# Optimization experiments

Measured on AMD Instinct MI355X. Metric: run time of the kernel, lower is better.

Reference implementation:

```python
import jax, jax.numpy as jnp
import numpy as np

B, P, C = 64, 8732, 81
NEG_POS_RATIO = 3


def _smooth_l1_masked_sum(p, t, maskf):
    # smooth_l1 with beta=1, sum reduction, restricted to positive priors
    d = jnp.abs(p - t)
    l = jnp.where(d < 1.0, 0.5 * d * d, d - 0.5)  # [B,P,K]
    return jnp.sum(l.sum(-1) * maskf)


def setup_inputs() -> dict:
    key = jax.random.key(0)
    ks = jax.random.split(key, 6)
    loc_data = jax.random.normal(ks[0], (B, P, 4), jnp.float32)
    conf_data = jax.random.normal(ks[1], (B, P, C), jnp.float32)
    four_corners_data = jax.random.normal(ks[2], (B, P, 8), jnp.float32)
    loc_t = jax.random.normal(ks[3], (B, P, 4), jnp.float32)
    four_corners_t = jax.random.normal(ks[4], (B, P, 8), jnp.float32)
    conf_t = jax.random.randint(ks[5], (B, P), 0, C, jnp.int32)
    return {
        "loc_data": loc_data,
        "conf_data": conf_data,
        "four_corners_data": four_corners_data,
        "loc_t": loc_t,
        "four_corners_t": four_corners_t,
        "conf_t": conf_t,
    }


def reference(loc_data, conf_data, four_corners_data, loc_t, four_corners_t, conf_t):
    num_priors = conf_data.shape[1]
    pos = conf_t > 0                                  # [B,P]
    posf = pos.astype(conf_data.dtype)

    # localization + four-corner smooth-L1 over matched (positive) priors
    loss_l = _smooth_l1_masked_sum(loc_data, loc_t, posf)
    loss_four_corners = _smooth_l1_masked_sum(four_corners_data, four_corners_t, posf)

    # per-prior CE loss: log_sum_exp(conf) - conf[target]
    lse = jax.nn.logsumexp(conf_data, axis=-1)        # [B,P]
    gathered = jnp.take_along_axis(conf_data, conf_t[..., None], axis=-1)[..., 0]
    ce_all = lse - gathered                           # [B,P]

    # hard-negative mining: rank negatives by CE loss (double argsort)
    loss_c_mine = jnp.where(pos, 0.0, ce_all)
    loss_idx = jnp.argsort(-loss_c_mine, axis=1)      # descending sort indices
    idx_rank = jnp.argsort(loss_idx, axis=1)          # rank of each prior
    num_pos = pos.sum(axis=1, keepdims=True)          # [B,1]
    num_neg = jnp.minimum(NEG_POS_RATIO * num_pos, num_priors - 1)
    neg = idx_rank < num_neg                          # [B,P]

    sel = pos | neg
    loss_c = jnp.sum(jnp.where(sel, ce_all, 0.0))

    N = num_pos.sum().astype(conf_data.dtype)
    return (loss_l / N, loss_c / N, loss_four_corners / N)
```

## Files before the change

### kernel.cpp

```cpp
#include <hip/hip_runtime.h>


#define NB 64
#define NP 8732
#define NC 81
constexpr int BP = NB * NP;
constexpr int PBLK = (NP + 255) / 256;
constexpr unsigned MAXCH = (unsigned)((size_t)BP * NC / 4 - 1);

__device__ inline float sl1(float d) {
    d = fabsf(d);
    return d < 1.0f ? 0.5f * d * d : d - 0.5f;
}


__global__ __launch_bounds__(256) void k_main(
    const float* __restrict__ loc_data, const float* __restrict__ conf_data,
    const float* __restrict__ fc_data,  const float* __restrict__ loc_t,
    const float* __restrict__ fc_t,     const int* __restrict__ conf_t,
    float* __restrict__ ce, float* __restrict__ part)
{
    const int b  = blockIdx.y;
    const int bx = blockIdx.x;
    const int t  = threadIdx.x;
    const int p0 = bx << 8;

    __shared__ int   tgt_s[256];
    __shared__ float red[4][5];

    float l_sum = 0.0f, f_sum = 0.0f, sp = 0.0f, sn = 0.0f;
    int np = 0;

    {
        const int p = p0 + t;
        int tgt = 0;
        if (p < NP) {
            const size_t g = (size_t)b * NP + p;
            tgt = conf_t[g];
            const float posf = (tgt > 0) ? 1.0f : 0.0f;
            np = (tgt > 0) ? 1 : 0;
            float4 a4  = ((const float4*)loc_data)[g];
            float4 a4t = ((const float4*)loc_t)[g];
            l_sum = (sl1(a4.x - a4t.x) + sl1(a4.y - a4t.y) +
                     sl1(a4.z - a4t.z) + sl1(a4.w - a4t.w)) * posf;
            float4 c0 = ((const float4*)fc_data)[2 * g];
            float4 c1 = ((const float4*)fc_data)[2 * g + 1];
            float4 d0 = ((const float4*)fc_t)[2 * g];
            float4 d1 = ((const float4*)fc_t)[2 * g + 1];
            f_sum = (sl1(c0.x - d0.x) + sl1(c0.y - d0.y) + sl1(c0.z - d0.z) + sl1(c0.w - d0.w) +
                     sl1(c1.x - d1.x) + sl1(c1.y - d1.y) + sl1(c1.z - d1.z) + sl1(c1.w - d1.w)) * posf;
        }
        tgt_s[t] = tgt;
    }
    __syncthreads();

    const int wave = t >> 6, lane = t & 63;
    const int grp = lane >> 2, sub = lane & 3;
    const float4* conf4 = (const float4*)conf_data;

    #pragma unroll 1
    for (int s = 0; s < 4; ++s) {
        const int pl = (wave << 6) + (s << 4) + grp;
        const int p  = p0 + pl;
        const int pe = min(p, NP - 1);
        const unsigned g  = (unsigned)b * NP + (unsigned)pe;
        const unsigned fb = g * (unsigned)NC;
        const int al      = (int)(fb & 3u);
        const unsigned c0 = fb >> 2;

        const int tgt = tgt_s[pl];
        float tv = 0.0f;
        if (sub == 0) tv = conf_data[fb + (unsigned)tgt];

        float e = 0.0f;
        #pragma unroll
        for (int k = 0; k < 6; ++k) {
            unsigned ch = c0 + (unsigned)(sub + 4 * k);
            ch = ch > MAXCH ? MAXCH : ch;
            const float4 v = conf4[ch];
            const int bi = 4 * (sub + 4 * k) - al;
            e += ((unsigned)(bi + 0) < 81u) ? __expf(v.x) : 0.0f;
            e += ((unsigned)(bi + 1) < 81u) ? __expf(v.y) : 0.0f;
            e += ((unsigned)(bi + 2) < 81u) ? __expf(v.z) : 0.0f;
            e += ((unsigned)(bi + 3) < 81u) ? __expf(v.w) : 0.0f;
        }
        e += __shfl_xor(e, 1, 64);
        e += __shfl_xor(e, 2, 64);

        if (sub == 0 && p < NP) {
            const float cev = __logf(e) - tv;
            ce[g] = cev;
            if (tgt > 0) sp += cev; else sn += cev;
        }
    }

    float vnp = (float)np;
    #pragma unroll
    for (int o = 32; o; o >>= 1) {
        l_sum += __shfl_xor(l_sum, o, 64);
        f_sum += __shfl_xor(f_sum, o, 64);
        sp    += __shfl_xor(sp, o, 64);
        sn    += __shfl_xor(sn, o, 64);
        vnp   += __shfl_xor(vnp, o, 64);
    }
    if (lane == 0) {
        red[wave][0] = l_sum; red[wave][1] = f_sum;
        red[wave][2] = sp;    red[wave][3] = sn;   red[wave][4] = vnp;
    }
    __syncthreads();
    if (t == 0) {
        float rl = 0, rf = 0, rp = 0, rn = 0, rc = 0;
        #pragma unroll
        for (int w = 0; w < 4; ++w) {
            rl += red[w][0]; rf += red[w][1]; rp += red[w][2];
            rn += red[w][3]; rc += red[w][4];
        }
        float* pp = part + ((size_t)b * PBLK + bx) * 5;
        pp[0] = rl; pp[1] = rf; pp[2] = rp; pp[3] = rn; pp[4] = rc;
    }
}

__global__ __launch_bounds__(256) void k_batch(
    const float* __restrict__ ce, const int* __restrict__ conf_t,
    const float* __restrict__ part, float* __restrict__ loss_c_b,
    int* __restrict__ npos_b, float* __restrict__ lsum_b, float* __restrict__ fsum_b)
{
    const int b = blockIdx.x;
    const int t = threadIdx.x;
    __shared__ float hdr[3];

    if (t < 64) {
        float v0 = 0, v1 = 0, v2 = 0, v3 = 0, v4 = 0;
        if (t < PBLK) {
            const float* pp = part + ((size_t)b * PBLK + t) * 5;
            v0 = pp[0]; v1 = pp[1]; v2 = pp[2]; v3 = pp[3]; v4 = pp[4];
        }
        #pragma unroll
        for (int o = 32; o; o >>= 1) {
            v0 += __shfl_xor(v0, o, 64);
            v1 += __shfl_xor(v1, o, 64);
            v2 += __shfl_xor(v2, o, 64);
            v3 += __shfl_xor(v3, o, 64);
            v4 += __shfl_xor(v4, o, 64);
        }
        if (t == 0) {
            lsum_b[b] = v0; fsum_b[b] = v1;
            npos_b[b] = (int)v4;
            hdr[0] = v2; hdr[1] = v3; hdr[2] = v4;
        }
    }
    __syncthreads();

    const float spos = hdr[0], sneg = hdr[1];
    const int npos    = (int)hdr[2];
    const int nneg    = NP - npos;
    const int num_neg = min(3 * npos, NP - 1);

    if (num_neg >= nneg) {
        if (t == 0) loss_c_b[b] = spos + sneg;
        return;
    }
    if (num_neg <= 0) {
        if (t == 0) loss_c_b[b] = spos;
        return;
    }

    __shared__ float ce_s[NP];
    __shared__ float sredf[4];
    __shared__ int   sredi[4];
    const float* crow = ce + (size_t)b * NP;
    const int*   trow = conf_t + (size_t)b * NP;
    for (int p = t; p < NP; p += 256)
        ce_s[p] = (trow[p] > 0) ? -1.0f : crow[p];
    __syncthreads();

    const int wave = t >> 6, lane = t & 63;
    const int K = num_neg;
    unsigned lo = 0u, hi = 0x7f800000u;
    while (lo < hi) {
        unsigned mid = lo + ((hi - lo) >> 1);
        float v = __uint_as_float(mid);
        int c_t = 0;
        for (int p = t; p < NP; p += 256) c_t += (ce_s[p] > v) ? 1 : 0;
        #pragma unroll
        for (int o = 32; o; o >>= 1) c_t += __shfl_xor(c_t, o, 64);
        __syncthreads();
        if (lane == 0) sredi[wave] = c_t;
        __syncthreads();
        int cnt = sredi[0] + sredi[1] + sredi[2] + sredi[3];
        if (cnt < K) hi = mid; else lo = mid + 1;
    }
    float v = __uint_as_float(lo);
    int c_t = 0; float s_t = 0.0f;
    for (int p = t; p < NP; p += 256) {
        float x = ce_s[p];
        if (x > v) { c_t++; s_t += x; }
    }
    #pragma unroll
    for (int o = 32; o; o >>= 1) {
        c_t += __shfl_xor(c_t, o, 64);
        s_t += __shfl_xor(s_t, o, 64);
    }
    __syncthreads();
    if (lane == 0) { sredi[wave] = c_t; sredf[wave] = s_t; }
    __syncthreads();
    if (t == 0) {
        int   cnt = sredi[0] + sredi[1] + sredi[2] + sredi[3];
        float sgt = sredf[0] + sredf[1] + sredf[2] + sredf[3];
        loss_c_b[b] = spos + sgt + (float)(K - cnt) * v;
    }
}

__global__ void k_final(const float* __restrict__ loss_c_b,
                        const int* __restrict__ npos_b,
                        const float* __restrict__ lsum_b,
                        const float* __restrict__ fsum_b,
                        float* __restrict__ out)
{
    const int t = threadIdx.x;
    float lc = loss_c_b[t];
    float ls = lsum_b[t];
    float fs = fsum_b[t];
    int   np = npos_b[t];
    #pragma unroll
    for (int o = 32; o; o >>= 1) {
        lc += __shfl_xor(lc, o, 64);
        ls += __shfl_xor(ls, o, 64);
        fs += __shfl_xor(fs, o, 64);
        np += __shfl_xor(np, o, 64);
    }
    if (t == 0) {
        float N = (float)np;
        out[0] = ls / N;
        out[1] = lc / N;
        out[2] = fs / N;
    }
}

extern "C" void kernel_launch(void* const* d_in, const int* in_sizes, int n_in,
                              void* d_out, int out_size, void* d_ws, size_t ws_size,
                              hipStream_t stream)
{
    const float* loc_data  = (const float*)d_in[0];
    const float* conf_data = (const float*)d_in[1];
    const float* fc_data   = (const float*)d_in[2];
    const float* loc_t     = (const float*)d_in[3];
    const float* fc_t      = (const float*)d_in[4];
    const int*   conf_t    = (const int*)d_in[5];
    float* out = (float*)d_out;

    float* ce       = (float*)d_ws;
    float* part     = ce + BP;
    float* loss_c_b = part + NB * PBLK * 5;
    int*   npos_b   = (int*)(loss_c_b + 64);
    float* lsum_b   = (float*)(npos_b + 64);
    float* fsum_b   = lsum_b + 64;

    hipLaunchKernelGGL(k_main,  dim3(PBLK, NB), dim3(256), 0, stream,
                       loc_data, conf_data, fc_data, loc_t, fc_t, conf_t,
                       ce, part);
    hipLaunchKernelGGL(k_batch, dim3(NB), dim3(256), 0, stream,
                       ce, conf_t, part, loss_c_b, npos_b, lsum_b, fsum_b);
    hipLaunchKernelGGL(k_final, dim3(1), dim3(64), 0, stream,
                       loss_c_b, npos_b, lsum_b, fsum_b, out);
}
```

Measured before the change: 305.2 us.

## Split smooth-L1 and CE into separate kernels, double-buffer conf loads

The fused main kernel becomes two kernels: one for the smooth-L1 sums and positive count, one for per-prior cross-entropy. The CE kernel uses double-buffered register prefetch of the conf rows so loads for the next sub-tile are in flight while the current one is computed. It also takes the target logit from the already-loaded vectors instead of doing a separate scalar gather. The cost is an extra kernel launch, more registers, and reading conf_t twice.

```diff
diff --git a/kernel.cpp b/kernel.cpp
--- a/kernel.cpp
+++ b/kernel.cpp
@@ -14,116 +14,158 @@
 }
 
 
-__global__ __launch_bounds__(256) void k_main(
-    const float* __restrict__ loc_data, const float* __restrict__ conf_data,
-    const float* __restrict__ fc_data,  const float* __restrict__ loc_t,
-    const float* __restrict__ fc_t,     const int* __restrict__ conf_t,
-    float* __restrict__ ce, float* __restrict__ part)
+__global__ __launch_bounds__(256) void k_sl1(
+    const float* __restrict__ loc_data, const float* __restrict__ fc_data,
+    const float* __restrict__ loc_t,    const float* __restrict__ fc_t,
+    const int* __restrict__ conf_t,     float* __restrict__ partS)
 {
     const int b  = blockIdx.y;
     const int bx = blockIdx.x;
     const int t  = threadIdx.x;
-    const int p0 = bx << 8;
-
-    __shared__ int   tgt_s[256];
-    __shared__ float red[4][5];
-
-    float l_sum = 0.0f, f_sum = 0.0f, sp = 0.0f, sn = 0.0f;
+    const int p  = (bx << 8) + t;
+
+    __shared__ float red[4][3];
+    float l_sum = 0.0f, f_sum = 0.0f;
     int np = 0;
 
-    {
-        const int p = p0 + t;
-        int tgt = 0;
-        if (p < NP) {
-            const size_t g = (size_t)b * NP + p;
-            tgt = conf_t[g];
-            const float posf = (tgt > 0) ? 1.0f : 0.0f;
-            np = (tgt > 0) ? 1 : 0;
-            float4 a4  = ((const float4*)loc_data)[g];
-            float4 a4t = ((const float4*)loc_t)[g];
-            l_sum = (sl1(a4.x - a4t.x) + sl1(a4.y - a4t.y) +
-                     sl1(a4.z - a4t.z) + sl1(a4.w - a4t.w)) * posf;
-            float4 c0 = ((const float4*)fc_data)[2 * g];
-            float4 c1 = ((const float4*)fc_data)[2 * g + 1];
-            float4 d0 = ((const float4*)fc_t)[2 * g];
-            float4 d1 = ((const float4*)fc_t)[2 * g + 1];
-            f_sum = (sl1(c0.x - d0.x) + sl1(c0.y - d0.y) + sl1(c0.z - d0.z) + sl1(c0.w - d0.w) +
-                     sl1(c1.x - d1.x) + sl1(c1.y - d1.y) + sl1(c1.z - d1.z) + sl1(c1.w - d1.w)) * posf;
-        }
-        tgt_s[t] = tgt;
-    }
-    __syncthreads();
+    if (p < NP) {
+        const size_t g = (size_t)b * NP + p;
+        const int tgt = conf_t[g];
+        const float posf = (tgt > 0) ? 1.0f : 0.0f;
+        np = (tgt > 0) ? 1 : 0;
+        float4 a4  = ((const float4*)loc_data)[g];
+        float4 a4t = ((const float4*)loc_t)[g];
+        float4 c0  = ((const float4*)fc_data)[2 * g];
+        float4 c1  = ((const float4*)fc_data)[2 * g + 1];
+        float4 d0  = ((const float4*)fc_t)[2 * g];
+        float4 d1  = ((const float4*)fc_t)[2 * g + 1];
+        l_sum = (sl1(a4.x - a4t.x) + sl1(a4.y - a4t.y) +
+                 sl1(a4.z - a4t.z) + sl1(a4.w - a4t.w)) * posf;
+        f_sum = (sl1(c0.x - d0.x) + sl1(c0.y - d0.y) + sl1(c0.z - d0.z) + sl1(c0.w - d0.w) +
+                 sl1(c1.x - d1.x) + sl1(c1.y - d1.y) + sl1(c1.z - d1.z) + sl1(c1.w - d1.w)) * posf;
+    }
 
     const int wave = t >> 6, lane = t & 63;
-    const int grp = lane >> 2, sub = lane & 3;
-    const float4* conf4 = (const float4*)conf_data;
-
-    #pragma unroll 1
-    for (int s = 0; s < 4; ++s) {
-        const int pl = (wave << 6) + (s << 4) + grp;
-        const int p  = p0 + pl;
-        const int pe = min(p, NP - 1);
-        const unsigned g  = (unsigned)b * NP + (unsigned)pe;
-        const unsigned fb = g * (unsigned)NC;
-        const int al      = (int)(fb & 3u);
-        const unsigned c0 = fb >> 2;
-
-        const int tgt = tgt_s[pl];
-        float tv = 0.0f;
-        if (sub == 0) tv = conf_data[fb + (unsigned)tgt];
-
-        float e = 0.0f;
-        #pragma unroll
-        for (int k = 0; k < 6; ++k) {
-            unsigned ch = c0 + (unsigned)(sub + 4 * k);
-            ch = ch > MAXCH ? MAXCH : ch;
-            const float4 v = conf4[ch];
-            const int bi = 4 * (sub + 4 * k) - al;
-            e += ((unsigned)(bi + 0) < 81u) ? __expf(v.x) : 0.0f;
-            e += ((unsigned)(bi + 1) < 81u) ? __expf(v.y) : 0.0f;
-            e += ((unsigned)(bi + 2) < 81u) ? __expf(v.z) : 0.0f;
-            e += ((unsigned)(bi + 3) < 81u) ? __expf(v.w) : 0.0f;
-        }
-        e += __shfl_xor(e, 1, 64);
-        e += __shfl_xor(e, 2, 64);
-
-        if (sub == 0 && p < NP) {
-            const float cev = __logf(e) - tv;
-            ce[g] = cev;
-            if (tgt > 0) sp += cev; else sn += cev;
-        }
-    }
-
     float vnp = (float)np;
     #pragma unroll
     for (int o = 32; o; o >>= 1) {
         l_sum += __shfl_xor(l_sum, o, 64);
         f_sum += __shfl_xor(f_sum, o, 64);
-        sp    += __shfl_xor(sp, o, 64);
-        sn    += __shfl_xor(sn, o, 64);
         vnp   += __shfl_xor(vnp, o, 64);
     }
-    if (lane == 0) {
-        red[wave][0] = l_sum; red[wave][1] = f_sum;
-        red[wave][2] = sp;    red[wave][3] = sn;   red[wave][4] = vnp;
-    }
+    if (lane == 0) { red[wave][0] = l_sum; red[wave][1] = f_sum; red[wave][2] = vnp; }
     __syncthreads();
     if (t == 0) {
-        float rl = 0, rf = 0, rp = 0, rn = 0, rc = 0;
+        float rl = 0, rf = 0, rc = 0;
         #pragma unroll
-        for (int w = 0; w < 4; ++w) {
-            rl += red[w][0]; rf += red[w][1]; rp += red[w][2];
-            rn += red[w][3]; rc += red[w][4];
-        }
-        float* pp = part + ((size_t)b * PBLK + bx) * 5;
-        pp[0] = rl; pp[1] = rf; pp[2] = rp; pp[3] = rn; pp[4] = rc;
+        for (int w = 0; w < 4; ++w) { rl += red[w][0]; rf += red[w][1]; rc += red[w][2]; }
+        float* ps = partS + ((size_t)b * PBLK + bx) * 4;
+        ps[0] = rl; ps[1] = rf; ps[2] = rc;
+    }
+}
+
+#define CE_ISSUE(BUF, PV, FBV, S)                                        \
+    {                                                                    \
+        const int pl = (wave << 6) + ((S) << 4) + grp;                   \
+        const int p  = p0 + pl;                                          \
+        const int pe = min(p, NP - 1);                                   \
+        const unsigned g  = (unsigned)b * NP + (unsigned)pe;             \
+        const unsigned fb = g * (unsigned)NC;                            \
+        const unsigned c0 = fb >> 2;                                     \
+        PV = p; FBV = fb;                                                \
+        _Pragma("unroll")                                                \
+        for (int k = 0; k < 6; ++k) {                                    \
+            unsigned ch = c0 + (unsigned)(sub + 4 * k);                  \
+            ch = ch > MAXCH ? MAXCH : ch;                                \
+            BUF[k] = conf4[ch];                                         \
+        }                                                                \
+    }
+
+#define CE_COMPUTE(BUF, PV, FBV, S)                                      \
+    {                                                                    \
+        const int pl  = (wave << 6) + ((S) << 4) + grp;                  \
+        const int tgt = tgt_s[pl];                                       \
+        const int al  = (int)(FBV & 3u);                                 \
+        float e = 0.0f, tv = 0.0f;                                       \
+        _Pragma("unroll")                                                \
+        for (int k = 0; k < 6; ++k) {                                    \
+            const float4 v = BUF[k];                                     \
+            const int bi = 4 * (sub + 4 * k) - al;                       \
+            e  += ((unsigned)(bi + 0) < 81u) ? __expf(v.x) : 0.0f;       \
+            e  += ((unsigned)(bi + 1) < 81u) ? __expf(v.y) : 0.0f;       \
+            e  += ((unsigned)(bi + 2) < 81u) ? __expf(v.z) : 0.0f;       \
+            e  += ((unsigned)(bi + 3) < 81u) ? __expf(v.w) : 0.0f;       \
+            tv += (bi + 0 == tgt) ? v.x : 0.0f;                          \
+            tv += (bi + 1 == tgt) ? v.y : 0.0f;                          \
+            tv += (bi + 2 == tgt) ? v.z : 0.0f;                          \
+            tv += (bi + 3 == tgt) ? v.w : 0.0f;                          \
+        }                                                                \
+        e  += __shfl_xor(e, 1, 64);  e  += __shfl_xor(e, 2, 64);         \
+        tv += __shfl_xor(tv, 1, 64); tv += __shfl_xor(tv, 2, 64);        \
+        if (sub == 0 && PV < NP) {                                       \
+            const unsigned g = (unsigned)b * NP + (unsigned)PV;          \
+            const float cev = __logf(e) - tv;                            \
+            ce[g] = cev;                                                 \
+            if (tgt > 0) sp += cev; else sn += cev;                      \
+        }                                                                \
+    }
+
+__global__ __launch_bounds__(256) void k_ce(
+    const float* __restrict__ conf_data, const int* __restrict__ conf_t,
+    float* __restrict__ ce, float* __restrict__ partC)
+{
+    const int b  = blockIdx.y;
+    const int bx = blockIdx.x;
+    const int t  = threadIdx.x;
+    const int p0 = bx << 8;
+
+    __shared__ int   tgt_s[256];
+    __shared__ float red[4][2];
+
+    {
+        const int p = p0 + t;
+        tgt_s[t] = (p < NP) ? conf_t[(size_t)b * NP + p] : 0;
+    }
+    __syncthreads();
+
+    const int wave = t >> 6, lane = t & 63;
+    const int grp = lane >> 2, sub = lane & 3;
+    const float4* conf4 = (const float4*)conf_data;
+    float sp = 0.0f, sn = 0.0f;
+
+    float4 bufA[6], bufB[6];
+    int pA, pB; unsigned fbA, fbB;
+
+    CE_ISSUE(bufA, pA, fbA, 0);
+    CE_ISSUE(bufB, pB, fbB, 1);
+    CE_COMPUTE(bufA, pA, fbA, 0);
+    CE_ISSUE(bufA, pA, fbA, 2);
+    CE_COMPUTE(bufB, pB, fbB, 1);
+    CE_ISSUE(bufB, pB, fbB, 3);
+    CE_COMPUTE(bufA, pA, fbA, 2);
+    CE_COMPUTE(bufB, pB, fbB, 3);
+
+    #pragma unroll
+    for (int o = 32; o; o >>= 1) {
+        sp += __shfl_xor(sp, o, 64);
+        sn += __shfl_xor(sn, o, 64);
+    }
+    if (lane == 0) { red[wave][0] = sp; red[wave][1] = sn; }
+    __syncthreads();
+    if (t == 0) {
+        float rp = 0, rn = 0;
+        #pragma unroll
+        for (int w = 0; w < 4; ++w) { rp += red[w][0]; rn += red[w][1]; }
+        float* pc = partC + ((size_t)b * PBLK + bx) * 2;
+        pc[0] = rp; pc[1] = rn;
     }
 }
 
 __global__ __launch_bounds__(256) void k_batch(
     const float* __restrict__ ce, const int* __restrict__ conf_t,
-    const float* __restrict__ part, float* __restrict__ loss_c_b,
-    int* __restrict__ npos_b, float* __restrict__ lsum_b, float* __restrict__ fsum_b)
+    const float* __restrict__ partS, const float* __restrict__ partC,
+    float* __restrict__ loss_c_b, int* __restrict__ npos_b,
+    float* __restrict__ lsum_b, float* __restrict__ fsum_b)
 {
     const int b = blockIdx.x;
     const int t = threadIdx.x;
@@ -132,8 +174,10 @@
     if (t < 64) {
         float v0 = 0, v1 = 0, v2 = 0, v3 = 0, v4 = 0;
         if (t < PBLK) {
-            const float* pp = part + ((size_t)b * PBLK + t) * 5;
-            v0 = pp[0]; v1 = pp[1]; v2 = pp[2]; v3 = pp[3]; v4 = pp[4];
+            const float* ps = partS + ((size_t)b * PBLK + t) * 4;
+            v0 = ps[0]; v1 = ps[1]; v4 = ps[2];
+            const float* pc = partC + ((size_t)b * PBLK + t) * 2;
+            v2 = pc[0]; v3 = pc[1];
         }
         #pragma unroll
         for (int o = 32; o; o >>= 1) {
@@ -250,17 +294,19 @@
     float* out = (float*)d_out;
 
     float* ce       = (float*)d_ws;
-    float* part     = ce + BP;
-    float* loss_c_b = part + NB * PBLK * 5;
+    float* partS    = ce + BP;
+    float* partC    = partS + NB * PBLK * 4;
+    float* loss_c_b = partC + NB * PBLK * 2;
     int*   npos_b   = (int*)(loss_c_b + 64);
     float* lsum_b   = (float*)(npos_b + 64);
     float* fsum_b   = lsum_b + 64;
 
-    hipLaunchKernelGGL(k_main,  dim3(PBLK, NB), dim3(256), 0, stream,
-                       loc_data, conf_data, fc_data, loc_t, fc_t, conf_t,
-                       ce, part);
+    hipLaunchKernelGGL(k_sl1,  dim3(PBLK, NB), dim3(256), 0, stream,
+                       loc_data, fc_data, loc_t, fc_t, conf_t, partS);
+    hipLaunchKernelGGL(k_ce,   dim3(PBLK, NB), dim3(256), 0, stream,
+                       conf_data, conf_t, ce, partC);
     hipLaunchKernelGGL(k_batch, dim3(NB), dim3(256), 0, stream,
-                       ce, conf_t, part, loss_c_b, npos_b, lsum_b, fsum_b);
+                       ce, conf_t, partS, partC, loss_c_b, npos_b, lsum_b, fsum_b);
     hipLaunchKernelGGL(k_final, dim3(1), dim3(64), 0, stream,
                        loss_c_b, npos_b, lsum_b, fsum_b, out);
 }
```

Result: no change. 300.0 us (-1.7%).
